# Performance work log

Measured on AMD Instinct MI355X. Metric: run time of the kernel, lower is better.

Reference implementation:

```python
import jax, jax.numpy as jnp
import numpy as np

N = 50000      # nodes
E = 800000     # edges
IN = 256       # in_feats
H = 128        # out_classes*2
OUT = 64       # out_classes
ALPHA = 0.3


def setup_inputs() -> dict:
    key = jax.random.key(0)
    ks = jax.random.split(key, 12)
    x = jax.random.normal(ks[0], (N, IN), jnp.float32)
    edge_index = jax.random.randint(ks[1], (2, E), 0, N, dtype=jnp.int32)
    def lin(k, fi, fo):
        s = 1.0 / np.float32(np.sqrt(fi))
        kw, kb = jax.random.split(k)
        return (jax.random.uniform(kw, (fi, fo), jnp.float32, -s, s),
                jax.random.uniform(kb, (fo,), jnp.float32, -s, s))
    W1, b1 = lin(ks[2], IN, H)
    W2, b2 = lin(ks[3], H, H)
    W3, b3 = lin(ks[4], H, H)
    Wfc, bfc = lin(ks[5], H, OUT)
    jk_weights = jax.random.normal(ks[6], (3,), jnp.float32)
    return dict(x=x, edge_index=edge_index, W1=W1, b1=b1, W2=W2, b2=b2,
                W3=W3, b3=b3, jk_weights=jk_weights, Wfc=Wfc, bfc=bfc)


def _gcn(x, W, b, src, dst, norm, n):
    # symmetric-normalized GCN conv with self-loops folded into src/dst/norm
    h = x @ W
    return jax.ops.segment_sum(norm[:, None] * h[src], dst, num_segments=n) + b


def reference(x, edge_index, W1, b1, W2, b2, W3, b3, jk_weights, Wfc, bfc):
    n = x.shape[0]
    row, col = edge_index[0], edge_index[1]
    loops = jnp.arange(n, dtype=edge_index.dtype)
    src = jnp.concatenate([row, loops])
    dst = jnp.concatenate([col, loops])
    deg = jax.ops.segment_sum(jnp.ones(src.shape, jnp.float32), dst, num_segments=n)
    dinv = jax.lax.rsqrt(jnp.maximum(deg, 1.0))  # deg >= 1 due to self-loops
    norm = dinv[src] * dinv[dst]

    layer_out = []
    # layer 0 + neighbor sampling (defaults make it exact out-neighbor mean)
    h = jax.nn.relu(_gcn(x, W1, b1, src, dst, norm, n))
    odeg = jax.ops.segment_sum(jnp.ones(row.shape, jnp.float32), row, num_segments=n)
    nsum = jax.ops.segment_sum(h[col], row, num_segments=n)
    h = jnp.where(odeg[:, None] > 0, nsum / jnp.maximum(odeg, 1.0)[:, None], h)
    layer_out.append(h)

    # layer 1 + historical EMA (fresh hist = detached x -> value identity, grad*alpha)
    h = jax.nn.relu(_gcn(h, W2, b2, src, dst, norm, n))
    sg = jax.lax.stop_gradient(h)
    h = sg + ALPHA * (h - sg)
    layer_out.append(h)

    # layer 2
    h = jax.nn.relu(_gcn(h, W3, b3, src, dst, norm, n))
    layer_out.append(h)

    w = jax.nn.softmax(jk_weights)
    jk = w[0] * layer_out[0] + w[1] * layer_out[1] + w[2] * layer_out[2]
    return jk @ Wfc + bfc
```

## Files before the change

### kernel.cpp

```cpp
#include <hip/hip_runtime.h>
#include <hip/hip_bf16.h>


#define H_FEATS 128
#define TPAD 136

typedef __attribute__((ext_vector_type(8))) short short8;
typedef __attribute__((ext_vector_type(4))) float float4v;
typedef unsigned short u16;

__device__ __forceinline__ float dload(const void* p, size_t i, int isbf) {
    return isbf ? __bfloat162float(((const __hip_bfloat16*)p)[i])
                : ((const float*)p)[i];
}

__device__ __forceinline__ float4 load4bf(const u16* p) {
    uint2 u = *(const uint2*)p;
    float4 f;
    f.x = __uint_as_float((u.x & 0xFFFFu) << 16);
    f.y = __uint_as_float(u.x & 0xFFFF0000u);
    f.z = __uint_as_float((u.y & 0xFFFFu) << 16);
    f.w = __uint_as_float(u.y & 0xFFFF0000u);
    return f;
}

__device__ __forceinline__ float bf2f(u16 h) {
    return __uint_as_float((unsigned)h << 16);
}

__device__ __forceinline__ u16 f2bf(float v) {
    return __bfloat16_as_ushort(__float2bfloat16(v));
}

__device__ __forceinline__ void add8(float* a, uint4 u) {
    a[0] += __uint_as_float((u.x & 0xFFFFu) << 16);
    a[1] += __uint_as_float(u.x & 0xFFFF0000u);
    a[2] += __uint_as_float((u.y & 0xFFFFu) << 16);
    a[3] += __uint_as_float(u.y & 0xFFFF0000u);
    a[4] += __uint_as_float((u.z & 0xFFFFu) << 16);
    a[5] += __uint_as_float(u.z & 0xFFFF0000u);
    a[6] += __uint_as_float((u.w & 0xFFFFu) << 16);
    a[7] += __uint_as_float(u.w & 0xFFFF0000u);
}

__device__ __forceinline__ void set8(float* a, uint4 u) {
    a[0] = __uint_as_float((u.x & 0xFFFFu) << 16);
    a[1] = __uint_as_float(u.x & 0xFFFF0000u);
    a[2] = __uint_as_float((u.y & 0xFFFFu) << 16);
    a[3] = __uint_as_float(u.y & 0xFFFF0000u);
    a[4] = __uint_as_float((u.z & 0xFFFFu) << 16);
    a[5] = __uint_as_float(u.z & 0xFFFF0000u);
    a[6] = __uint_as_float((u.w & 0xFFFFu) << 16);
    a[7] = __uint_as_float(u.w & 0xFFFF0000u);
}

__device__ __forceinline__ uint4 pack8(const float* f) {
    uint4 r;
    r.x = (unsigned)f2bf(f[0]) | ((unsigned)f2bf(f[1]) << 16);
    r.y = (unsigned)f2bf(f[2]) | ((unsigned)f2bf(f[3]) << 16);
    r.z = (unsigned)f2bf(f[4]) | ((unsigned)f2bf(f[5]) << 16);
    r.w = (unsigned)f2bf(f[6]) | ((unsigned)f2bf(f[7]) << 16);
    return r;
}

__device__ __forceinline__ void sniff_body(const unsigned int* __restrict__ x,
                                           const void* __restrict__ jkwb,
                                           float* __restrict__ meta) {
    __shared__ int cnt[256];
    int t = threadIdx.x;
    int c = 0;
    for (int i = 0; i < 16; i++) {
        unsigned int w = x[t * 16 + i];
        unsigned int e = (w >> 7) & 0xFFu;
        c += (e >= 0x60u && e <= 0x8Fu) ? 1 : 0;
    }
    cnt[t] = c;
    __syncthreads();
    for (int s = 128; s > 0; s >>= 1) {
        if (t < s) cnt[t] += cnt[t + s];
        __syncthreads();
    }
    if (t == 0) {
        int isbf = (cnt[0] > 3000) ? 1 : 0;
        ((int*)meta)[0] = isbf;
        float w0 = dload(jkwb, 0, isbf);
        float w1 = dload(jkwb, 1, isbf);
        float w2 = dload(jkwb, 2, isbf);
        float m = fmaxf(w0, fmaxf(w1, w2));
        float e0 = expf(w0 - m), e1 = expf(w1 - m), e2 = expf(w2 - m);
        float s = e0 + e1 + e2;
        meta[8] = e0 / s; meta[9] = e1 / s; meta[10] = e2 / s;
    }
}

__global__ __launch_bounds__(256) void sniff_jkw(const unsigned int* __restrict__ x,
                                                 const void* __restrict__ jkwb,
                                                 float* __restrict__ meta) {
    sniff_body(x, jkwb, meta);
}

#define CSR_CH 64
#define CSR_SL 8
#define CSR_NSC (CSR_CH * CSR_SL * 2)

__global__ __launch_bounds__(256) void count_partial(const int* __restrict__ row,
                                                     const int* __restrict__ col,
                                                     unsigned* __restrict__ partC,
                                                     unsigned* __restrict__ partR,
                                                     int E, int N,
                                                     const unsigned int* __restrict__ x,
                                                     const void* __restrict__ jkwb,
                                                     float* __restrict__ meta) {
    if (blockIdx.x == gridDim.x - 1) {
        sniff_body(x, jkwb, meta);
        return;
    }
    int b = blockIdx.x;
    int dir = b >> 9;
    int r = b & 511;
    int sl = r >> 6;
    int k  = r & 63;
    const int* arr = dir ? row : col;
    unsigned* part = (dir ? partR : partC) + (size_t)k * N;
    int lo = (int)(((long long)N * sl) >> 3);
    int hi = (int)(((long long)N * (sl + 1)) >> 3);
    int wid = hi - lo;

    __shared__ unsigned cnt[8192];
    for (int i = threadIdx.x; i < wid; i += 256) cnt[i] = 0;
    __syncthreads();

    int e0 = (int)(((long long)E * k) >> 6);
    int e1 = (int)(((long long)E * (k + 1)) >> 6);
    for (int e = e0 + threadIdx.x; e < e1; e += 256) {
        int d = arr[e] - lo;
        if ((unsigned)d < (unsigned)wid) atomicAdd(&cnt[d], 1u);
    }
    __syncthreads();
    for (int i = threadIdx.x; i < wid; i += 256) part[lo + i] = cnt[i];
}

__global__ __launch_bounds__(256) void reduce_bsum(const unsigned* __restrict__ partC,
                                                   const unsigned* __restrict__ partR,
                                                   int* __restrict__ cntc,
                                                   int* __restrict__ cntr,
                                                   int* __restrict__ b0,
                                                   int* __restrict__ b1, int N) {
    const unsigned* p = blockIdx.y ? partR : partC;
    int* cnt = blockIdx.y ? cntr : cntc;
    int* bs = blockIdx.y ? b1 : b0;
    int base = blockIdx.x * 1024 + threadIdx.x * 4;
    unsigned v0 = 0, v1 = 0, v2 = 0, v3 = 0;
    if (base + 3 < N) {
        for (int k = 0; k < CSR_CH; k++) {
            uint4 u = *(const uint4*)(p + (size_t)k * N + base);
            v0 += u.x; v1 += u.y; v2 += u.z; v3 += u.w;
        }
        int4 w = {(int)v0, (int)v1, (int)v2, (int)v3};
        *(int4*)&cnt[base] = w;
    } else {
        unsigned vv[4] = {0, 0, 0, 0};
        for (int k = 0; k < CSR_CH; k++)
            for (int i = 0; i < 4; i++)
                if (base + i < N) vv[i] += p[(size_t)k * N + base + i];
        for (int i = 0; i < 4; i++) if (base + i < N) cnt[base + i] = (int)vv[i];
        v0 = vv[0]; v1 = vv[1]; v2 = vv[2]; v3 = vv[3];
    }
    int s = (int)(v0 + v1 + v2 + v3);
    __shared__ int red[256];
    red[threadIdx.x] = s;
    __syncthreads();
    for (int d = 128; d > 0; d >>= 1) {
        if (threadIdx.x < d) red[threadIdx.x] += red[threadIdx.x + d];
        __syncthreads();
    }
    if (threadIdx.x == 0) bs[blockIdx.x] = red[0];
}

__device__ __forceinline__ void scatter_body(int b,
                                             const int* __restrict__ row,
                                             const int* __restrict__ col,
                                             const unsigned* __restrict__ partC,
                                             const unsigned* __restrict__ partR,
                                             u16* __restrict__ ecol,
                                             u16* __restrict__ erow,
                                             int E, int N,
                                             unsigned* __restrict__ cur) {
    int dir = b >> 9;
    int r = b & 511;
    int sl = r >> 6;
    int k  = r & 63;
    const int* darr = dir ? row : col;
    const int* sarr = dir ? col : row;
    u16* out = dir ? erow : ecol;
    const unsigned* base = (dir ? partR : partC) + (size_t)k * N;
    int lo = (int)(((long long)N * sl) >> 3);
    int hi = (int)(((long long)N * (sl + 1)) >> 3);
    int wid = hi - lo;

    for (int i = threadIdx.x; i < wid; i += 256) cur[i] = base[lo + i];
    __syncthreads();

    int e0 = (int)(((long long)E * k) >> 6);
    int e1 = (int)(((long long)E * (k + 1)) >> 6);
    for (int e = e0 + threadIdx.x; e < e1; e += 256) {
        int d = darr[e] - lo;
        if ((unsigned)d < (unsigned)wid) {
            unsigned p = atomicAdd(&cur[d], 1u);
            out[p] = (u16)sarr[e];
        }
    }
}

__global__ __launch_bounds__(256) void histo_sniff(const int* __restrict__ row, const int* __restrict__ col,
                                                   int* __restrict__ cntc, int* __restrict__ cntr, int E,
                                                   const unsigned int* __restrict__ x,
                                                   const void* __restrict__ jkwb,
                                                   float* __restrict__ meta) {
    if (blockIdx.x == gridDim.x - 1) {
        sniff_body(x, jkwb, meta);
        return;
    }
    int e = blockIdx.x * 256 + threadIdx.x;
    if (e < E) {
        atomicAdd(&cntc[col[e]], 1);
        atomicAdd(&cntr[row[e]], 1);
    }
}

__global__ __launch_bounds__(256) void scan_bsum(const int* __restrict__ c0, const int* __restrict__ c1,
                                                 int* __restrict__ b0, int* __restrict__ b1, int N) {
    const int* cnt = blockIdx.y ? c1 : c0;
    int* bs = blockIdx.y ? b1 : b0;
    int base = blockIdx.x * 1024 + threadIdx.x * 4;
    int s = 0;
    if (base + 3 < N) {
        int4 v = *(const int4*)&cnt[base];
        s = v.x + v.y + v.z + v.w;
    } else {
        for (int i = 0; i < 4; i++) if (base + i < N) s += cnt[base + i];
    }
    __shared__ int red[256];
    red[threadIdx.x] = s;
    __syncthreads();
    for (int d = 128; d > 0; d >>= 1) {
        if (threadIdx.x < d) red[threadIdx.x] += red[threadIdx.x + d];
        __syncthreads();
    }
    if (threadIdx.x == 0) bs[blockIdx.x] = red[0];
}

__global__ __launch_bounds__(256) void scan_bsum_scan(int* __restrict__ b0, int* __restrict__ b1,
                                                      int* __restrict__ offN0, int* __restrict__ offN1,
                                                      int nb) {
    int* bs = blockIdx.x ? b1 : b0;
    int* offN = blockIdx.x ? offN1 : offN0;
    __shared__ int sh[256];
    int t = threadIdx.x;
    int v = (t < nb) ? bs[t] : 0;
    sh[t] = v;
    __syncthreads();
    for (int d = 1; d < 256; d <<= 1) {
        int u = (t >= d) ? sh[t - d] : 0;
        __syncthreads();
        sh[t] += u;
        __syncthreads();
    }
    if (t < nb) bs[t] = (t == 0) ? 0 : sh[t - 1];
    if (t == 255) *offN = sh[255];
}

__global__ __launch_bounds__(256) void scan_final(const int* __restrict__ c0, const int* __restrict__ c1,
                                                  const int* __restrict__ b0, const int* __restrict__ b1,
                                                  int* __restrict__ o0, int* __restrict__ u0,
                                                  int* __restrict__ o1, int* __restrict__ u1,
                                                  unsigned* __restrict__ pc,
                                                  unsigned* __restrict__ pr,
                                                  float* __restrict__ dinvp, int N) {
    const int* cnt = blockIdx.y ? c1 : c0;
    const int* bs  = blockIdx.y ? b1 : b0;
    int* off = blockIdx.y ? o1 : o0;
    int* cur = blockIdx.y ? u1 : u0;
    unsigned* part = blockIdx.y ? pr : pc;
    int t = threadIdx.x;
    int base = blockIdx.x * 1024 + t * 4;
    int4 v = {0, 0, 0, 0};
    if (base + 3 < N) {
        v = *(const int4*)&cnt[base];
    } else {
        int tmp[4] = {0, 0, 0, 0};
        for (int i = 0; i < 4; i++) if (base + i < N) tmp[i] = cnt[base + i];
        v.x = tmp[0]; v.y = tmp[1]; v.z = tmp[2]; v.w = tmp[3];
    }
    if (blockIdx.y == 0) {
        if (base + 3 < N) {
            float4 dv;
            dv.x = rsqrtf(1.0f + (float)v.x);
            dv.y = rsqrtf(1.0f + (float)v.y);
            dv.z = rsqrtf(1.0f + (float)v.z);
            dv.w = rsqrtf(1.0f + (float)v.w);
            *(float4*)&dinvp[base] = dv;
        } else {
            int vv[4] = {v.x, v.y, v.z, v.w};
            for (int i = 0; i < 4; i++)
                if (base + i < N) dinvp[base + i] = rsqrtf(1.0f + (float)vv[i]);
        }
    }
    int s = v.x + v.y + v.z + v.w;
    __shared__ int sh[256];
    sh[t] = s;
    __syncthreads();
    for (int d = 1; d < 256; d <<= 1) {
        int u = (t >= d) ? sh[t - d] : 0;
        __syncthreads();
        sh[t] += u;
        __syncthreads();
    }
    int ex = bs[blockIdx.x] + ((t == 0) ? 0 : sh[t - 1]);
    int4 o;
    o.x = ex; o.y = ex + v.x; o.z = o.y + v.y; o.w = o.z + v.z;
    if (base + 3 < N) {
        *(int4*)&off[base] = o;
        *(int4*)&cur[base] = o;
        if (part) {
            unsigned a0 = (unsigned)o.x, a1 = (unsigned)o.y,
                     a2 = (unsigned)o.z, a3 = (unsigned)o.w;
            for (int k = 0; k < CSR_CH; k++) {
                unsigned* pp = part + (size_t)k * N + base;
                uint4 u = *(const uint4*)pp;
                uint4 w = {a0, a1, a2, a3};
                *(uint4*)pp = w;
                a0 += u.x; a1 += u.y; a2 += u.z; a3 += u.w;
            }
        }
    } else {
        int arr[4] = {o.x, o.y, o.z, o.w};
        for (int i = 0; i < 4; i++) if (base + i < N) { off[base + i] = arr[i]; cur[base + i] = arr[i]; }
        if (part) {
            for (int i = 0; i < 4; i++) {
                if (base + i >= N) continue;
                unsigned acc = (unsigned)arr[i];
                for (int k = 0; k < CSR_CH; k++) {
                    unsigned* pp = part + (size_t)k * N + base + i;
                    unsigned tv = *pp;
                    *pp = acc;
                    acc += tv;
                }
            }
        }
    }
}

__global__ __launch_bounds__(256) void scatter_tile(const int* __restrict__ row, const int* __restrict__ col,
                                                    int* __restrict__ curc, int* __restrict__ curr,
                                                    u16* __restrict__ ecol, u16* __restrict__ erow,
                                                    int E, int lo, int hi, int doRow) {
    int e = blockIdx.x * 256 + threadIdx.x;
    if (e >= E) return;
    int s = row[e], d = col[e];
    if (d >= lo && d < hi) {
        int p = atomicAdd(&curc[d], 1);
        ecol[p] = (u16)s;
    }
    if (doRow && s >= lo && s < hi) {
        int q = atomicAdd(&curr[s], 1);
        erow[q] = (u16)d;
    }
}

__global__ __launch_bounds__(256) void pack_all(const void* __restrict__ W1,
                                                const void* __restrict__ W2,
                                                const void* __restrict__ W3,
                                                const void* __restrict__ Wf,
                                                u16* __restrict__ Wp1,
                                                u16* __restrict__ Wp2,
                                                u16* __restrict__ Wp3,
                                                u16* __restrict__ Wfp,
                                                const int* __restrict__ flagp) {
    int bid = blockIdx.x;
    const void* W; u16* Wp; int K, C, gid;
    if (bid < 16)      { W = W1; Wp = Wp1; K = 256; C = 128; gid = bid * 256 + threadIdx.x; }
    else if (bid < 24) { W = W2; Wp = Wp2; K = 128; C = 128; gid = (bid - 16) * 256 + threadIdx.x; }
    else if (bid < 32) { W = W3; Wp = Wp3; K = 128; C = 128; gid = (bid - 24) * 256 + threadIdx.x; }
    else               { W = Wf; Wp = Wfp; K = 128; C = 64;  gid = (bid - 32) * 256 + threadIdx.x; }
    int tiles = C >> 4;
    int steps = K >> 5;
    if (gid >= steps * tiles * 64) return;
    int isbf = *flagp;
    int lane = gid & 63;
    int tt = (gid >> 6) % tiles;
    int s = (gid >> 6) / tiles;
    int krow = s * 32 + ((lane >> 4) << 3);
    int ncol = tt * 16 + (lane & 15);
#pragma unroll
    for (int j = 0; j < 8; j++) {
        float v = dload(W, (size_t)(krow + j) * C + ncol, isbf);
        Wp[(size_t)gid * 8 + j] = f2bf(v);
    }
}

template <int K, bool RTBF, bool BFIN, bool SCALE>
__device__ __forceinline__ void gemm_mfma_body(int bid, const void* __restrict__ Xv,
                                               const u16* __restrict__ Wp,
                                               u16* __restrict__ Cb,
                                               const float* __restrict__ dinv,
                                               const int* __restrict__ flagp, int M) {
    const int isbf = RTBF ? *flagp : (BFIN ? 1 : 0);
    const int tid = threadIdx.x;
    const int wave = tid >> 6, lane = tid & 63;
    const int m16 = lane & 15, quad = lane >> 4;
    const int row = bid * 64 + wave * 16 + m16;
    constexpr int STEPS = K / 32;

    float4v acc[8];
#pragma unroll
    for (int t = 0; t < 8; t++) acc[t] = (float4v){0.f, 0.f, 0.f, 0.f};

    const bool rowOK = row < M;
#pragma unroll
    for (int s = 0; s < STEPS; s++) {
        int k0 = s * 32 + quad * 8;
        short8 a = (short8)(short)0;
        if (rowOK) {
            if (isbf) {
                a = *(const short8*)((const u16*)Xv + (size_t)row * K + k0);
            } else {
                const float* p = (const float*)Xv + (size_t)row * K + k0;
                float4 f0 = *(const float4*)p;
                float4 f1 = *(const float4*)(p + 4);
                a[0] = (short)f2bf(f0.x); a[1] = (short)f2bf(f0.y);
                a[2] = (short)f2bf(f0.z); a[3] = (short)f2bf(f0.w);
                a[4] = (short)f2bf(f1.x); a[5] = (short)f2bf(f1.y);
                a[6] = (short)f2bf(f1.z); a[7] = (short)f2bf(f1.w);
            }
        }
#pragma unroll
        for (int t = 0; t < 8; t++) {
            short8 b = *(const short8*)(Wp + ((size_t)(s * 8 + t) * 64 + lane) * 8);
            acc[t] = __builtin_amdgcn_mfma_f32_16x16x32_bf16(a, b, acc[t], 0, 0, 0);
        }
    }
#pragma unroll
    for (int r = 0; r < 4; r++) {
        int gr = bid * 64 + wave * 16 + quad * 4 + r;
        if (gr < M) {
            float sc = SCALE ? dinv[gr] : 1.0f;
#pragma unroll
            for (int t = 0; t < 8; t++) {
                size_t o = (size_t)gr * H_FEATS + t * 16 + m16;
                Cb[o] = f2bf(sc * acc[t][r]);
            }
        }
    }
}

template <int K, bool RTBF, bool BFIN, bool SCALE>
__global__ __launch_bounds__(256) void gemm_mfma(const void* __restrict__ Xv,
                                                 const u16* __restrict__ Wp,
                                                 u16* __restrict__ Cb,
                                                 const float* __restrict__ dinv,
                                                 const int* __restrict__ flagp, int M) {
    gemm_mfma_body<K, RTBF, BFIN, SCALE>(blockIdx.x, Xv, Wp, Cb, dinv, flagp, M);
}

__global__ __launch_bounds__(256) void scatter_gemm0(const int* __restrict__ row,
                                                     const int* __restrict__ col,
                                                     const unsigned* __restrict__ partC,
                                                     const unsigned* __restrict__ partR,
                                                     u16* __restrict__ ecol,
                                                     u16* __restrict__ erow,
                                                     int E, int N,
                                                     const void* __restrict__ Xv,
                                                     const u16* __restrict__ Wp,
                                                     u16* __restrict__ Pb,
                                                     const float* __restrict__ dinv,
                                                     const int* __restrict__ flagp) {
    __shared__ unsigned cur[8192];
    if (blockIdx.x < CSR_NSC) {
        scatter_body(blockIdx.x, row, col, partC, partR, ecol, erow, E, N, cur);
    } else {
        gemm_mfma_body<256, true, false, true>(blockIdx.x - CSR_NSC, Xv, Wp, Pb, dinv, flagp, N);
    }
}

__global__ __launch_bounds__(256) void agg_sum(const int* __restrict__ off,
                                               const u16* __restrict__ idx,
                                               const float* __restrict__ dinv,
                                               const u16* __restrict__ Pb,
                                               const void* __restrict__ bv,
                                               u16* __restrict__ hout,
                                               const int* __restrict__ flagp, int N) {
    int node = blockIdx.x * 8 + (threadIdx.x >> 5);
    if (node >= N) return;
    int l = threadIdx.x & 31;
    int isbf = *flagp;
    int beg = off[node], end = off[node + 1];
    size_t ro = (size_t)l * 4;

    float4 acc = load4bf(&Pb[(size_t)node * H_FEATS + ro]);

    const float4 z = {0.f, 0.f, 0.f, 0.f};
    int i = beg;
    int s0 = (i     < end) ? (int)idx[i]     : 0;
    int s1 = (i + 1 < end) ? (int)idx[i + 1] : 0;
    int s2 = (i + 2 < end) ? (int)idx[i + 2] : 0;
    int s3 = (i + 3 < end) ? (int)idx[i + 3] : 0;
    float4 h0 = (i     < end) ? load4bf(&Pb[(size_t)s0 * H_FEATS + ro]) : z;
    float4 h1 = (i + 1 < end) ? load4bf(&Pb[(size_t)s1 * H_FEATS + ro]) : z;
    float4 h2 = (i + 2 < end) ? load4bf(&Pb[(size_t)s2 * H_FEATS + ro]) : z;
    float4 h3 = (i + 3 < end) ? load4bf(&Pb[(size_t)s3 * H_FEATS + ro]) : z;
    for (; i + 4 < end; i += 4) {
        int t0 = (int)idx[i + 4];
        int t1 = (i + 5 < end) ? (int)idx[i + 5] : 0;
        int t2 = (i + 6 < end) ? (int)idx[i + 6] : 0;
        int t3 = (i + 7 < end) ? (int)idx[i + 7] : 0;
        float4 n0 = load4bf(&Pb[(size_t)t0 * H_FEATS + ro]);
        float4 n1 = (i + 5 < end) ? load4bf(&Pb[(size_t)t1 * H_FEATS + ro]) : z;
        float4 n2 = (i + 6 < end) ? load4bf(&Pb[(size_t)t2 * H_FEATS + ro]) : z;
        float4 n3 = (i + 7 < end) ? load4bf(&Pb[(size_t)t3 * H_FEATS + ro]) : z;
        acc.x += (h0.x + h1.x) + (h2.x + h3.x);
        acc.y += (h0.y + h1.y) + (h2.y + h3.y);
        acc.z += (h0.z + h1.z) + (h2.z + h3.z);
        acc.w += (h0.w + h1.w) + (h2.w + h3.w);
        h0 = n0; h1 = n1; h2 = n2; h3 = n3;
    }
    acc.x += (h0.x + h1.x) + (h2.x + h3.x);
    acc.y += (h0.y + h1.y) + (h2.y + h3.y);
    acc.z += (h0.z + h1.z) + (h2.z + h3.z);
    acc.w += (h0.w + h1.w) + (h2.w + h3.w);

    float dd = dinv[node];
    acc.x = fmaxf(fmaf(dd, acc.x, dload(bv, l * 4 + 0, isbf)), 0.0f);
    acc.y = fmaxf(fmaf(dd, acc.y, dload(bv, l * 4 + 1, isbf)), 0.0f);
    acc.z = fmaxf(fmaf(dd, acc.z, dload(bv, l * 4 + 2, isbf)), 0.0f);
    acc.w = fmaxf(fmaf(dd, acc.w, dload(bv, l * 4 + 3, isbf)), 0.0f);
    uint2 pk;
    pk.x = (unsigned)f2bf(acc.x) | ((unsigned)f2bf(acc.y) << 16);
    pk.y = (unsigned)f2bf(acc.z) | ((unsigned)f2bf(acc.w) << 16);
    *(uint2*)&hout[(size_t)node * H_FEATS + ro] = pk;
}

template <int MODE, bool WRITEG>
__device__ __forceinline__ void gather_tile(int bid,
                                            const int* __restrict__ off,
                                            const u16* __restrict__ idx,
                                            const float* __restrict__ dinv,
                                            const u16* __restrict__ Src,
                                            const void* __restrict__ bv, int isbf,
                                            u16* __restrict__ Hg,
                                            u16* __restrict__ tile, int N) {
    int lane16 = threadIdx.x & 15;
    int rloc = threadIdx.x >> 4;
    int co = lane16 * 8;
    const uint4 zz = {0u, 0u, 0u, 0u};
#pragma unroll
    for (int pass = 0; pass < 4; ++pass) {
        int r = pass * 16 + rloc;
        int gr = bid * 64 + r;
        uint4* ldst = (uint4*)(tile + (size_t)r * TPAD + co);
        if (gr >= N) { *ldst = zz; continue; }
        int beg = off[gr], end = off[gr + 1];
        float acc[8];
        if (MODE == 0) {
            uint4 u = *(const uint4*)(Src + (size_t)gr * H_FEATS + co);
            set8(acc, u);
        } else {
#pragma unroll
            for (int j = 0; j < 8; j++) acc[j] = 0.0f;
        }
        int i = beg;
        int s0 = (i     < end) ? (int)idx[i]     : 0;
        int s1 = (i + 1 < end) ? (int)idx[i + 1] : 0;
        int s2 = (i + 2 < end) ? (int)idx[i + 2] : 0;
        int s3 = (i + 3 < end) ? (int)idx[i + 3] : 0;
        uint4 h0 = (i     < end) ? *(const uint4*)(Src + (size_t)s0 * H_FEATS + co) : zz;
        uint4 h1 = (i + 1 < end) ? *(const uint4*)(Src + (size_t)s1 * H_FEATS + co) : zz;
        uint4 h2 = (i + 2 < end) ? *(const uint4*)(Src + (size_t)s2 * H_FEATS + co) : zz;
        uint4 h3 = (i + 3 < end) ? *(const uint4*)(Src + (size_t)s3 * H_FEATS + co) : zz;
        for (; i + 4 < end; i += 4) {
            int t0 = (int)idx[i + 4];
            int t1 = (i + 5 < end) ? (int)idx[i + 5] : 0;
            int t2 = (i + 6 < end) ? (int)idx[i + 6] : 0;
            int t3 = (i + 7 < end) ? (int)idx[i + 7] : 0;
            uint4 n0 = *(const uint4*)(Src + (size_t)t0 * H_FEATS + co);
            uint4 n1 = (i + 5 < end) ? *(const uint4*)(Src + (size_t)t1 * H_FEATS + co) : zz;
            uint4 n2 = (i + 6 < end) ? *(const uint4*)(Src + (size_t)t2 * H_FEATS + co) : zz;
            uint4 n3 = (i + 7 < end) ? *(const uint4*)(Src + (size_t)t3 * H_FEATS + co) : zz;
            add8(acc, h0); add8(acc, h1); add8(acc, h2); add8(acc, h3);
            h0 = n0; h1 = n1; h2 = n2; h3 = n3;
        }
        add8(acc, h0); add8(acc, h1); add8(acc, h2); add8(acc, h3);

        if (MODE == 0) {
            float dd = dinv[gr];
#pragma unroll
            for (int j = 0; j < 8; j++)
                acc[j] = fmaxf(fmaf(dd, acc[j], dload(bv, co + j, isbf)), 0.0f);
        } else {
            int cnt = end - beg;
            if (cnt > 0) {
                float inv = 1.0f / (float)cnt;
#pragma unroll
                for (int j = 0; j < 8; j++) acc[j] *= inv;
            } else {
                uint4 u = *(const uint4*)(Src + (size_t)gr * H_FEATS + co);
                set8(acc, u);
            }
        }
        uint4 pk = pack8(acc);
        *ldst = pk;
        if (WRITEG) *(uint4*)(Hg + (size_t)gr * H_FEATS + co) = pk;
    }
}

__device__ __forceinline__ void gemm_lds_body(int bid, const u16* __restrict__ tile,
                                              const u16* __restrict__ Wp,
                                              u16* __restrict__ Cb,
                                              const float* __restrict__ dinv, int M) {
    const int tid = threadIdx.x;
    const int wave = tid >> 6, lane = tid & 63;
    const int m16 = lane & 15, quad = lane >> 4;
    const int lrow = wave * 16 + m16;

    float4v acc[8];
#pragma unroll
    for (int t = 0; t < 8; t++) acc[t] = (float4v){0.f, 0.f, 0.f, 0.f};

#pragma unroll
    for (int s = 0; s < 4; s++) {
        int k0 = s * 32 + quad * 8;
        short8 a = *(const short8*)(tile + (size_t)lrow * TPAD + k0);
#pragma unroll
        for (int t = 0; t < 8; t++) {
            short8 b = *(const short8*)(Wp + ((size_t)(s * 8 + t) * 64 + lane) * 8);
            acc[t] = __builtin_amdgcn_mfma_f32_16x16x32_bf16(a, b, acc[t], 0, 0, 0);
        }
    }
#pragma unroll
    for (int r = 0; r < 4; r++) {
        int gr = bid * 64 + wave * 16 + quad * 4 + r;
        if (gr < M) {
            float sc = dinv[gr];
#pragma unroll
            for (int t = 0; t < 8; t++) {
                size_t o = (size_t)gr * H_FEATS + t * 16 + m16;
                Cb[o] = f2bf(sc * acc[t][r]);
            }
        }
    }
}

template <int MODE>
__global__ __launch_bounds__(256) void agg_gemm(const int* __restrict__ off,
                                                const u16* __restrict__ idx,
                                                const float* __restrict__ dinv,
                                                const u16* __restrict__ Src,
                                                const void* __restrict__ bv,
                                                const u16* __restrict__ Wp,
                                                u16* __restrict__ Hg,
                                                u16* __restrict__ Pnext,
                                                const int* __restrict__ flagp, int N) {
    __shared__ u16 tile[64 * TPAD];
    gather_tile<MODE, true>(blockIdx.x, off, idx, dinv, Src, bv, *flagp, Hg, tile, N);
    __syncthreads();
    gemm_lds_body(blockIdx.x, tile, Wp, Pnext, dinv, N);
}

__global__ __launch_bounds__(256) void agg_fc3(const int* __restrict__ off,
                                               const u16* __restrict__ idx,
                                               const float* __restrict__ dinv,
                                               const u16* __restrict__ Src,
                                               const void* __restrict__ bv3,
                                               const u16* __restrict__ H0,
                                               const u16* __restrict__ H1,
                                               const u16* __restrict__ Wfp,
                                               const void* __restrict__ bv,
                                               void* __restrict__ Outv,
                                               const float* __restrict__ meta, int N) {
    __shared__ u16 tile[64 * TPAD];
    const int isbf = ((const int*)meta)[0];
    gather_tile<0, false>(blockIdx.x, off, idx, dinv, Src, bv3, isbf, (u16*)0, tile, N);
    __syncthreads();

    const float w0 = meta[8], w1 = meta[9], w2 = meta[10];
    const int tid = threadIdx.x;
    const int wave = tid >> 6, lane = tid & 63;
    const int m16 = lane & 15, quad = lane >> 4;
    const int lrow = wave * 16 + m16;
    const int gr0 = blockIdx.x * 64 + lrow;

    float4v acc[4];
#pragma unroll
    for (int t = 0; t < 4; t++) acc[t] = (float4v){0.f, 0.f, 0.f, 0.f};

#pragma unroll
    for (int s = 0; s < 4; s++) {
        int k0 = s * 32 + quad * 8;
        short8 a = (short8)(short)0;
        if (gr0 < N) {
            float f0[8], f1[8], f2[8];
            uint4 u0 = *(const uint4*)(H0 + (size_t)gr0 * H_FEATS + k0);
            uint4 u1 = *(const uint4*)(H1 + (size_t)gr0 * H_FEATS + k0);
            uint4 tv = *(const uint4*)(tile + (size_t)lrow * TPAD + k0);
            set8(f0, u0); set8(f1, u1); set8(f2, tv);
#pragma unroll
            for (int j = 0; j < 8; j++)
                a[j] = (short)f2bf(w0 * f0[j] + w1 * f1[j] + w2 * f2[j]);
        }
#pragma unroll
        for (int t = 0; t < 4; t++) {
            short8 b = *(const short8*)(Wfp + ((size_t)(s * 4 + t) * 64 + lane) * 8);
            acc[t] = __builtin_amdgcn_mfma_f32_16x16x32_bf16(a, b, acc[t], 0, 0, 0);
        }
    }

    __hip_bfloat16* ob = (__hip_bfloat16*)Outv;
    float* of = (float*)Outv;
#pragma unroll
    for (int r = 0; r < 4; r++) {
        int gr = blockIdx.x * 64 + wave * 16 + quad * 4 + r;
        if (gr < N) {
#pragma unroll
            for (int t = 0; t < 4; t++) {
                int c = t * 16 + m16;
                size_t o = (size_t)gr * 64 + c;
                float v = acc[t][r] + dload(bv, c, isbf);
                if (isbf) ob[o] = __float2bfloat16(v); else of[o] = v;
            }
        }
    }
}

template <bool BF16OUT>
__global__ __launch_bounds__(256) void agg_gather3b(const int* __restrict__ off,
                                                    const u16* __restrict__ idx,
                                                    const float* __restrict__ dinv,
                                                    const u16* __restrict__ Hb,
                                                    const void* __restrict__ bv,
                                                    void* __restrict__ houtv,
                                                    const int* __restrict__ flagp, int N) {
    int node = blockIdx.x * 8 + (threadIdx.x >> 5);
    if (node >= N) return;
    int l = threadIdx.x & 31;
    int isbf = *flagp;
    int beg = off[node], end = off[node + 1];
    float dd = dinv[node];
    size_t ro = (size_t)l * 4;

    float4 self = load4bf(&Hb[(size_t)node * H_FEATS + ro]);
    float w0s = dd * dd;
    float4 acc = {w0s * self.x, w0s * self.y, w0s * self.z, w0s * self.w};

    int i = beg;
    int s0 = (i < end) ? (int)idx[i] : 0;
    float4 h0 = (i < end) ? load4bf(&Hb[(size_t)s0 * H_FEATS + ro])
                          : (float4){0.f, 0.f, 0.f, 0.f};
    for (; i < end; i++) {
        int s1 = (i + 1 < end) ? (int)idx[i + 1] : 0;
        float4 h1 = (i + 1 < end) ? load4bf(&Hb[(size_t)s1 * H_FEATS + ro]) : h0;
        float w = dinv[s0] * dd;
        acc.x = fmaf(w, h0.x, acc.x);
        acc.y = fmaf(w, h0.y, acc.y);
        acc.z = fmaf(w, h0.z, acc.z);
        acc.w = fmaf(w, h0.w, acc.w);
        s0 = s1; h0 = h1;
    }
    acc.x = fmaxf(acc.x + dload(bv, l * 4 + 0, isbf), 0.0f);
    acc.y = fmaxf(acc.y + dload(bv, l * 4 + 1, isbf), 0.0f);
    acc.z = fmaxf(acc.z + dload(bv, l * 4 + 2, isbf), 0.0f);
    acc.w = fmaxf(acc.w + dload(bv, l * 4 + 3, isbf), 0.0f);
    if (BF16OUT) {
        u16* hb = (u16*)houtv;
        uint2 pk;
        pk.x = (unsigned)f2bf(acc.x) | ((unsigned)f2bf(acc.y) << 16);
        pk.y = (unsigned)f2bf(acc.z) | ((unsigned)f2bf(acc.w) << 16);
        *(uint2*)&hb[(size_t)node * H_FEATS + ro] = pk;
    } else {
        *(float4*)&((float*)houtv)[(size_t)node * H_FEATS + ro] = acc;
    }
}

template <int K, bool XIN, bool GATEBF, bool BF16OUT>
__global__ __launch_bounds__(256) void gemm128(const void* __restrict__ Xv,
                                               const void* __restrict__ Wv,
                                               void* __restrict__ Cv,
                                               const int* __restrict__ flagp, int N) {
    constexpr int BM = 64, BK = 16, BN = 128, TN = 8, TX = BN / TN;
    __shared__ float Xs[BK][BM + 4];
    __shared__ float Ws[BK][BN];
    const int isbf = *flagp;
    if (GATEBF && isbf != 1) return;
    const float* Xf = (const float*)Xv;

    const int tid = threadIdx.x;
    const int tx = tid % TX;
    const int ty = tid / TX;
    const int rowBase = blockIdx.x * BM;

    float acc[4][TN] = {};
    const int lk = tid % BK;
    const int lr0 = tid / BK;

    for (int kb = 0; kb < K; kb += BK) {
#pragma unroll
        for (int i = 0; i < 4; i++) {
            int r = lr0 + i * 16;
            int gr = rowBase + r;
            float v = 0.0f;
            if (gr < N) {
                size_t idx = (size_t)gr * K + kb + lk;
                v = XIN ? dload(Xv, idx, isbf) : Xf[idx];
            }
            Xs[lk][r] = v;
        }
#pragma unroll
        for (int i = 0; i < 8; i++) {
            int idx = i * 256 + tid;
            int k = idx >> 7, c = idx & 127;
            Ws[k][c] = dload(Wv, (size_t)(kb + k) * BN + c, isbf);
        }
        __syncthreads();
#pragma unroll
        for (int k = 0; k < BK; k++) {
            float4 a = *(const float4*)&Xs[k][ty * 4];
            float av[4] = {a.x, a.y, a.z, a.w};
            float4 b0 = *(const float4*)&Ws[k][tx * TN];
            float4 b1 = *(const float4*)&Ws[k][tx * TN + 4];
            float bv[8] = {b0.x, b0.y, b0.z, b0.w, b1.x, b1.y, b1.z, b1.w};
#pragma unroll
            for (int i = 0; i < 4; i++)
#pragma unroll
                for (int j = 0; j < TN; j++) acc[i][j] = fmaf(av[i], bv[j], acc[i][j]);
        }
        __syncthreads();
    }
#pragma unroll
    for (int i = 0; i < 4; i++) {
        int gr = rowBase + ty * 4 + i;
        if (gr < N) {
#pragma unroll
            for (int j = 0; j < TN; j++) {
                size_t o = (size_t)gr * BN + tx * TN + j;
                if (BF16OUT) ((u16*)Cv)[o] = f2bf(acc[i][j]);
                else         ((float*)Cv)[o] = acc[i][j];
            }
        }
    }
}

template <bool FIRST, bool LAST, bool BFIN>
__global__ __launch_bounds__(256) void fc_accum(const void* __restrict__ Hmv,
                                                const void* __restrict__ Wv,
                                                const void* __restrict__ bv,
                                                void* __restrict__ Outv,
                                                const float* __restrict__ meta,
                                                int widx, int N) {
    constexpr int BM = 64, BK = 16, BN = 64, TN = 4, TX = BN / TN, K = 128;
    __shared__ float Xs[BK][BM + 4];
    __shared__ float Ws[BK][BN];
    const int isbf = ((const int*)meta)[0];
    const float scale = meta[8 + widx];

    const int tid = threadIdx.x;
    const int tx = tid % TX;
    const int ty = tid / TX;
    const int rowBase = blockIdx.x * BM;

    float acc[4][TN] = {};
    const int lk = tid % BK;
    const int lr0 = tid / BK;

    for (int kb = 0; kb < K; kb += BK) {
#pragma unroll
        for (int i = 0; i < 4; i++) {
            int r = lr0 + i * 16;
            int gr = rowBase + r;
            float v = 0.0f;
            if (gr < N) {
                size_t idx = (size_t)gr * K + kb + lk;
                if (BFIN) v = bf2f(((const u16*)Hmv)[idx]);
                else      v = ((const float*)Hmv)[idx];
            }
            Xs[lk][r] = v;
        }
#pragma unroll
        for (int i = 0; i < 4; i++) {
            int idx = i * 256 + tid;
            int k = idx >> 6, c = idx & 63;
            Ws[k][c] = dload(Wv, (size_t)(kb + k) * BN + c, isbf);
        }
        __syncthreads();
#pragma unroll
        for (int k = 0; k < BK; k++) {
            float4 a = *(const float4*)&Xs[k][ty * 4];
            float av[4] = {a.x, a.y, a.z, a.w};
            float4 bb = *(const float4*)&Ws[k][tx * TN];
            float bvv[4] = {bb.x, bb.y, bb.z, bb.w};
#pragma unroll
            for (int i = 0; i < 4; i++)
#pragma unroll
                for (int j = 0; j < TN; j++) acc[i][j] = fmaf(av[i], bvv[j], acc[i][j]);
        }
        __syncthreads();
    }
    __hip_bfloat16* ob = (__hip_bfloat16*)Outv;
    float* of = (float*)Outv;
#pragma unroll
    for (int i = 0; i < 4; i++) {
        int gr = rowBase + ty * 4 + i;
        if (gr < N) {
#pragma unroll
            for (int j = 0; j < TN; j++) {
                int c = tx * TN + j;
                size_t o = (size_t)gr * BN + c;
                float v = scale * acc[i][j];
                if (!FIRST) v += isbf ? __bfloat162float(ob[o]) : of[o];
                if (LAST) v += dload(bv, c, isbf);
                if (isbf) ob[o] = __float2bfloat16(v); else of[o] = v;
            }
        }
    }
}

__global__ __launch_bounds__(256) void init_deg(float* deg, float* odeg, int N) {
    int i = blockIdx.x * 256 + threadIdx.x;
    if (i < N) { deg[i] = 1.0f; odeg[i] = 0.0f; }
}
__global__ __launch_bounds__(256) void count_deg(const int* __restrict__ row, const int* __restrict__ col,
                                                 float* deg, float* odeg, int E) {
    int e = blockIdx.x * 256 + threadIdx.x;
    if (e < E) {
        atomicAdd(&deg[col[e]], 1.0f);
        atomicAdd(&odeg[row[e]], 1.0f);
    }
}
__global__ __launch_bounds__(256) void deg_to_dinv(float* deg, int N) {
    int i = blockIdx.x * 256 + threadIdx.x;
    if (i < N) deg[i] = rsqrtf(deg[i]);
}
__global__ __launch_bounds__(256) void agg_edges(const int* __restrict__ row, const int* __restrict__ col,
                                                 const float* __restrict__ dinv,
                                                 const float* __restrict__ H,
                                                 float* __restrict__ agg, int E) {
    int e = blockIdx.x * 2 + (threadIdx.x >> 7);
    if (e >= E) return;
    int j = threadIdx.x & 127;
    int s = row[e], d = col[e];
    float w = dinv[s] * dinv[d];
    atomicAdd(&agg[(size_t)d * H_FEATS + j], w * H[(size_t)s * H_FEATS + j]);
}
__global__ __launch_bounds__(256) void mean_edges(const int* __restrict__ row, const int* __restrict__ col,
                                                  const float* __restrict__ h0pre,
                                                  float* __restrict__ nsum, int E) {
    int e = blockIdx.x * 2 + (threadIdx.x >> 7);
    if (e >= E) return;
    int j = threadIdx.x & 127;
    int r = row[e], c = col[e];
    atomicAdd(&nsum[(size_t)r * H_FEATS + j], h0pre[(size_t)c * H_FEATS + j]);
}
__global__ __launch_bounds__(256) void finalize_layer(const float* __restrict__ agg,
                                                      const float* __restrict__ H,
                                                      const float* __restrict__ dinv,
                                                      const void* __restrict__ bv,
                                                      float* __restrict__ hout,
                                                      const int* __restrict__ flagp, int NH) {
    int idx = blockIdx.x * 256 + threadIdx.x;
    if (idx >= NH) return;
    int isbf = *flagp;
    int v = idx >> 7, j = idx & 127;
    float di = dinv[v];
    float h = fmaf(di * di, H[idx], agg[idx]) + dload(bv, j, isbf);
    hout[idx] = fmaxf(h, 0.0f);
}
__global__ __launch_bounds__(256) void finalize_mean(const float* __restrict__ nsum,
                                                     const float* __restrict__ h0pre,
                                                     const float* __restrict__ odeg,
                                                     float* __restrict__ h0, int NH) {
    int idx = blockIdx.x * 256 + threadIdx.x;
    if (idx >= NH) return;
    int v = idx >> 7;
    float od = odeg[v];
    h0[idx] = (od > 0.0f) ? (nsum[idx] / od) : h0pre[idx];
}
__global__ __launch_bounds__(256) void finalize_mean_cnt(const float* __restrict__ nsum,
                                                         const float* __restrict__ h0pre,
                                                         const int* __restrict__ cntr,
                                                         float* __restrict__ h0, int NH) {
    int idx = blockIdx.x * 256 + threadIdx.x;
    if (idx >= NH) return;
    int v = idx >> 7;
    int od = cntr[v];
    h0[idx] = (od > 0) ? (nsum[idx] / (float)od) : h0pre[idx];
}

extern "C" void kernel_launch(void* const* d_in, const int* in_sizes, int n_in,
                              void* d_out, int out_size, void* d_ws, size_t ws_size,
                              hipStream_t stream) {
    const void* x   = d_in[0];
    const int*  ei  = (const int*)d_in[1];
    const void* W1  = d_in[2];
    const void* b1  = d_in[3];
    const void* W2  = d_in[4];
    const void* b2  = d_in[5];
    const void* W3  = d_in[6];
    const void* b3  = d_in[7];
    const void* jkb = d_in[8];
    const void* Wfc = d_in[9];
    const void* bfc = d_in[10];

    const int IN = 256;
    const int N = in_sizes[0] / IN;
    const int E = in_sizes[1] / 2;
    const int NH = N * H_FEATS;

    const int* row = ei;
    const int* col = ei + E;

    auto a4 = [](size_t v) { return (v + 3) & ~(size_t)3; };
    float* ws = (float*)d_ws;
    size_t o = 0;
    float* meta  = ws + o;           o += 256;
    float* dinv  = ws + o;           o += N;          o = a4(o);
    int*   cntc  = (int*)(ws + o);   o += N;          o = a4(o);
    int*   cntr  = (int*)(ws + o);   o += N;          o = a4(o);
    int*   bsumc = (int*)(ws + o);   o += 256;
    int*   bsumr = (int*)(ws + o);   o += 256;
    int*   coff  = (int*)(ws + o);   o += N + 1;      o = a4(o);
    int*   curc  = (int*)(ws + o);   o += N;          o = a4(o);
    u16*   ecol  = (u16*)(ws + o);   o += E;          o = a4(o);
    size_t oB_small = o;
    int*   roff  = (int*)(ws + o);   o += N + 1;      o = a4(o);
    int*   curr  = (int*)(ws + o);   o += N;          o = a4(o);
    u16*   erow  = (u16*)(ws + o);   o += E;          o = a4(o);
    size_t oA_full = o;

    auto alignup = [](size_t v) { return (v + 63) & ~(size_t)63; };
    const size_t WPW = 16384 + 8192 + 8192 + 4096;
    size_t needA = alignup(oA_full) + 2 * (size_t)NH + 64 + WPW;
    size_t needB = alignup(oB_small) + 2 * (size_t)NH + 64 + WPW;

    int tier;
    size_t hoff;
    if (N >= 65536)                { tier = 2; hoff = alignup(256 + 2 * (size_t)N); }
    else if (ws_size >= needA * 4) { tier = 0; hoff = alignup(oA_full); }
    else if (ws_size >= needB * 4) { tier = 1; hoff = alignup(oB_small); }
    else                           { tier = 2; hoff = alignup(256 + 2 * (size_t)N); }
    float* A = ws + hoff;
    float* B = A + NH;
    u16* HbA = (u16*)A;
    u16* HbB = (u16*)B;
    u16* Pb  = (u16*)A;
    u16* Qb  = Pb + (size_t)NH;
    u16* H0b = Pb + 2 * (size_t)NH;
    u16* H1b = Pb + 3 * (size_t)NH;
    unsigned* partC = (unsigned*)H0b;
    unsigned* partR = partC + (size_t)CSR_CH * N;
    size_t wpoff = alignup(hoff + 2 * (size_t)NH);
    u16* Wp1 = (u16*)(ws + wpoff);
    u16* Wp2 = Wp1 + 32768;
    u16* Wp3 = Wp2 + 16384;
    u16* Wfcp = Wp3 + 16384;
    float* odegf = ws + 256 + N;
    const int* flag = (const int*)meta;

    dim3 blk(256);
    int gN = (N + 255) / 256;
    int gE = (E + 255) / 256;
    int gE2 = (E + 1) / 2;
    int gNH = (NH + 255) / 256;
    int gGemm = (N + 63) / 64;
    int gNode8 = (N + 7) / 8;
    int nb = (N + 1023) / 1024;

    if (tier == 0) {
        count_partial<<<CSR_NSC + 1, blk, 0, stream>>>(row, col, partC, partR, E, N,
                                                       (const unsigned int*)x, jkb, meta);
        pack_all<<<36, blk, 0, stream>>>(W1, W2, W3, Wfc, Wp1, Wp2, Wp3, Wfcp, flag);
        reduce_bsum<<<dim3(nb, 2), blk, 0, stream>>>(partC, partR, cntc, cntr, bsumc, bsumr, N);
        scan_bsum_scan<<<2, blk, 0, stream>>>(bsumc, bsumr, &coff[N], &roff[N], nb);
        scan_final<<<dim3(nb, 2), blk, 0, stream>>>(cntc, cntr, bsumc, bsumr,
                                                    coff, curc, roff, curr,
                                                    partC, partR, dinv, N);

        scatter_gemm0<<<CSR_NSC + gGemm, blk, 0, stream>>>(row, col, partC, partR, ecol, erow,
                                                           E, N, x, Wp1, Pb, dinv, flag);

        agg_sum<<<gNode8, blk, 0, stream>>>(coff, ecol, dinv, Pb, b1, Qb, flag, N);

        agg_gemm<1><<<gGemm, blk, 0, stream>>>(roff, erow, dinv, Qb, b1, Wp2, H0b, Pb, flag, N);

        agg_gemm<0><<<gGemm, blk, 0, stream>>>(coff, ecol, dinv, Pb, b2, Wp3, H1b, Qb, flag, N);

        agg_fc3<<<gGemm, blk, 0, stream>>>(coff, ecol, dinv, Qb, b3, H0b, H1b,
                                           Wfcp, bfc, d_out, meta, N);
    } else if (tier == 1) {
        hipMemsetAsync(cntc, 0, 2 * (size_t)N * 4, stream);
        histo_sniff<<<gE + 1, blk, 0, stream>>>(row, col, cntc, cntr, E,
                                                (const unsigned int*)x, jkb, meta);
        const int T = 4;
        int step = (N + T - 1) / T;
        scan_bsum<<<dim3(nb, 1), blk, 0, stream>>>(cntc, cntc, bsumc, bsumc, N);
        scan_bsum_scan<<<1, blk, 0, stream>>>(bsumc, bsumc, &coff[N], &coff[N], nb);
        scan_final<<<dim3(nb, 1), blk, 0, stream>>>(cntc, cntc, bsumc, bsumc,
                                                    coff, curc, coff, curc,
                                                    (unsigned*)0, (unsigned*)0, dinv, N);
        for (int t = 0; t < T; t++) {
            int lo = t * step, hi = lo + step; if (hi > N) hi = N;
            scatter_tile<<<gE, blk, 0, stream>>>(row, col, curc, curc, ecol, ecol, E, lo, hi, 0);
        }

        pack_all<<<36, blk, 0, stream>>>(W1, W2, W3, Wfc, Wp1, Wp2, Wp3, Wfcp, flag);

        gemm_mfma<256, true, false, false><<<gGemm, blk, 0, stream>>>(x, Wp1, HbA, dinv, flag, N);
        agg_gather3b<false><<<gNode8, blk, 0, stream>>>(coff, ecol, dinv, HbA, b1, B, flag, N);
        hipMemsetAsync(A, 0, (size_t)NH * 4, stream);
        mean_edges<<<gE2, blk, 0, stream>>>(row, col, B, A, E);
        finalize_mean_cnt<<<gNH, blk, 0, stream>>>(A, B, cntr, A, NH);
        fc_accum<true, false, false><<<gGemm, blk, 0, stream>>>(A, Wfc, bfc, d_out, meta, 0, N);

        gemm_mfma<128, false, false, false><<<gGemm, blk, 0, stream>>>(A, Wp2, HbB, dinv, flag, N);
        agg_gather3b<true><<<gNode8, blk, 0, stream>>>(coff, ecol, dinv, HbB, b2, HbA, flag, N);
        fc_accum<false, false, true><<<gGemm, blk, 0, stream>>>(HbA, Wfc, bfc, d_out, meta, 1, N);

        gemm_mfma<128, false, true, false><<<gGemm, blk, 0, stream>>>(HbA, Wp3, HbB, dinv, flag, N);
        agg_gather3b<true><<<gNode8, blk, 0, stream>>>(coff, ecol, dinv, HbB, b3, HbA, flag, N);
        fc_accum<false, true, true><<<gGemm, blk, 0, stream>>>(HbA, Wfc, bfc, d_out, meta, 2, N);
    } else {
        sniff_jkw<<<1, blk, 0, stream>>>((const unsigned int*)x, jkb, meta);
        init_deg<<<gN, blk, 0, stream>>>(dinv, odegf, N);
        count_deg<<<gE, blk, 0, stream>>>(row, col, dinv, odegf, E);
        deg_to_dinv<<<gN, blk, 0, stream>>>(dinv, N);

        gemm128<256, true, false, false><<<gGemm, blk, 0, stream>>>(x, W1, A, flag, N);
        hipMemsetAsync(B, 0, (size_t)NH * 4, stream);
        agg_edges<<<gE2, blk, 0, stream>>>(row, col, dinv, A, B, E);
        finalize_layer<<<gNH, blk, 0, stream>>>(B, A, dinv, b1, B, flag, NH);
        hipMemsetAsync(A, 0, (size_t)NH * 4, stream);
        mean_edges<<<gE2, blk, 0, stream>>>(row, col, B, A, E);
        finalize_mean<<<gNH, blk, 0, stream>>>(A, B, odegf, A, NH);
        fc_accum<true, false, false><<<gGemm, blk, 0, stream>>>(A, Wfc, bfc, d_out, meta, 0, N);

        gemm128<128, false, false, false><<<gGemm, blk, 0, stream>>>(A, W2, B, flag, N);
        hipMemsetAsync(A, 0, (size_t)NH * 4, stream);
        agg_edges<<<gE2, blk, 0, stream>>>(row, col, dinv, B, A, E);
        finalize_layer<<<gNH, blk, 0, stream>>>(A, B, dinv, b2, A, flag, NH);
        fc_accum<false, false, false><<<gGemm, blk, 0, stream>>>(A, Wfc, bfc, d_out, meta, 1, N);

        gemm128<128, false, false, false><<<gGemm, blk, 0, stream>>>(A, W3, B, flag, N);
        hipMemsetAsync(A, 0, (size_t)NH * 4, stream);
        agg_edges<<<gE2, blk, 0, stream>>>(row, col, dinv, B, A, E);
        finalize_layer<<<gNH, blk, 0, stream>>>(A, B, dinv, b3, A, flag, NH);
        fc_accum<false, true, false><<<gGemm, blk, 0, stream>>>(A, Wfc, bfc, d_out, meta, 2, N);
    }
}
```

Baseline: 405.8 us.

## Halve fused gather-GEMM tile to 32 rows and size CSR LDS dynamically

```diff
diff --git a/kernel.cpp b/kernel.cpp
--- a/kernel.cpp
+++ b/kernel.cpp
@@ -115,6 +115,7 @@
         sniff_body(x, jkwb, meta);
         return;
     }
+    extern __shared__ unsigned cnt[];
     int b = blockIdx.x;
     int dir = b >> 9;
     int r = b & 511;
@@ -126,7 +127,6 @@
     int hi = (int)(((long long)N * (sl + 1)) >> 3);
     int wid = hi - lo;
 
-    __shared__ unsigned cnt[8192];
     for (int i = threadIdx.x; i < wid; i += 256) cnt[i] = 0;
     __syncthreads();
 
@@ -475,7 +475,7 @@
                                                      u16* __restrict__ Pb,
                                                      const float* __restrict__ dinv,
                                                      const int* __restrict__ flagp) {
-    __shared__ unsigned cur[8192];
+    extern __shared__ unsigned cur[];
     if (blockIdx.x < CSR_NSC) {
         scatter_body(blockIdx.x, row, col, partC, partR, ecol, erow, E, N, cur);
     } else {
@@ -554,9 +554,9 @@
     int co = lane16 * 8;
     const uint4 zz = {0u, 0u, 0u, 0u};
 #pragma unroll
-    for (int pass = 0; pass < 4; ++pass) {
+    for (int pass = 0; pass < 2; ++pass) {
         int r = pass * 16 + rloc;
-        int gr = bid * 64 + r;
+        int gr = bid * 32 + r;
         uint4* ldst = (uint4*)(tile + (size_t)r * TPAD + co);
         if (gr >= N) { *ldst = zz; continue; }
         int beg = off[gr], end = off[gr + 1];
@@ -613,37 +613,39 @@
     }
 }
 
-__device__ __forceinline__ void gemm_lds_body(int bid, const u16* __restrict__ tile,
-                                              const u16* __restrict__ Wp,
-                                              u16* __restrict__ Cb,
-                                              const float* __restrict__ dinv, int M) {
+__device__ __forceinline__ void gemm_lds_body32(int bid, const u16* __restrict__ tile,
+                                                const u16* __restrict__ Wp,
+                                                u16* __restrict__ Cb,
+                                                const float* __restrict__ dinv, int M) {
     const int tid = threadIdx.x;
     const int wave = tid >> 6, lane = tid & 63;
     const int m16 = lane & 15, quad = lane >> 4;
-    const int lrow = wave * 16 + m16;
-
-    float4v acc[8];
-#pragma unroll
-    for (int t = 0; t < 8; t++) acc[t] = (float4v){0.f, 0.f, 0.f, 0.f};
+    const int rg = wave & 1, cg = wave >> 1;
+    const int lrow = rg * 16 + m16;
+
+    float4v acc[4];
+#pragma unroll
+    for (int t = 0; t < 4; t++) acc[t] = (float4v){0.f, 0.f, 0.f, 0.f};
 
 #pragma unroll
     for (int s = 0; s < 4; s++) {
         int k0 = s * 32 + quad * 8;
         short8 a = *(const short8*)(tile + (size_t)lrow * TPAD + k0);
 #pragma unroll
-        for (int t = 0; t < 8; t++) {
-            short8 b = *(const short8*)(Wp + ((size_t)(s * 8 + t) * 64 + lane) * 8);
+        for (int t = 0; t < 4; t++) {
+            int tg = cg * 4 + t;
+            short8 b = *(const short8*)(Wp + ((size_t)(s * 8 + tg) * 64 + lane) * 8);
             acc[t] = __builtin_amdgcn_mfma_f32_16x16x32_bf16(a, b, acc[t], 0, 0, 0);
         }
     }
 #pragma unroll
     for (int r = 0; r < 4; r++) {
-        int gr = bid * 64 + wave * 16 + quad * 4 + r;
+        int gr = bid * 32 + rg * 16 + quad * 4 + r;
         if (gr < M) {
             float sc = dinv[gr];
 #pragma unroll
-            for (int t = 0; t < 8; t++) {
-                size_t o = (size_t)gr * H_FEATS + t * 16 + m16;
+            for (int t = 0; t < 4; t++) {
+                size_t o = (size_t)gr * H_FEATS + (cg * 4 + t) * 16 + m16;
                 Cb[o] = f2bf(sc * acc[t][r]);
             }
         }
@@ -660,10 +662,10 @@
                                                 u16* __restrict__ Hg,
                                                 u16* __restrict__ Pnext,
                                                 const int* __restrict__ flagp, int N) {
-    __shared__ u16 tile[64 * TPAD];
+    __shared__ u16 tile[32 * TPAD];
     gather_tile<MODE, true>(blockIdx.x, off, idx, dinv, Src, bv, *flagp, Hg, tile, N);
     __syncthreads();
-    gemm_lds_body(blockIdx.x, tile, Wp, Pnext, dinv, N);
+    gemm_lds_body32(blockIdx.x, tile, Wp, Pnext, dinv, N);
 }
 
 __global__ __launch_bounds__(256) void agg_fc3(const int* __restrict__ off,
@@ -677,7 +679,7 @@
                                                const void* __restrict__ bv,
                                                void* __restrict__ Outv,
                                                const float* __restrict__ meta, int N) {
-    __shared__ u16 tile[64 * TPAD];
+    __shared__ u16 tile[32 * TPAD];
     const int isbf = ((const int*)meta)[0];
     gather_tile<0, false>(blockIdx.x, off, idx, dinv, Src, bv3, isbf, (u16*)0, tile, N);
     __syncthreads();
@@ -686,12 +688,13 @@
     const int tid = threadIdx.x;
     const int wave = tid >> 6, lane = tid & 63;
     const int m16 = lane & 15, quad = lane >> 4;
-    const int lrow = wave * 16 + m16;
-    const int gr0 = blockIdx.x * 64 + lrow;
-
-    float4v acc[4];
-#pragma unroll
-    for (int t = 0; t < 4; t++) acc[t] = (float4v){0.f, 0.f, 0.f, 0.f};
+    const int rg = wave & 1, cg = wave >> 1;
+    const int lrow = rg * 16 + m16;
+    const int gr0 = blockIdx.x * 32 + lrow;
+
+    float4v acc[2];
+#pragma unroll
+    for (int t = 0; t < 2; t++) acc[t] = (float4v){0.f, 0.f, 0.f, 0.f};
 
 #pragma unroll
     for (int s = 0; s < 4; s++) {
@@ -708,8 +711,9 @@
                 a[j] = (short)f2bf(w0 * f0[j] + w1 * f1[j] + w2 * f2[j]);
         }
 #pragma unroll
-        for (int t = 0; t < 4; t++) {
-            short8 b = *(const short8*)(Wfp + ((size_t)(s * 4 + t) * 64 + lane) * 8);
+        for (int t = 0; t < 2; t++) {
+            int tg = cg * 2 + t;
+            short8 b = *(const short8*)(Wfp + ((size_t)(s * 4 + tg) * 64 + lane) * 8);
             acc[t] = __builtin_amdgcn_mfma_f32_16x16x32_bf16(a, b, acc[t], 0, 0, 0);
         }
     }
@@ -718,11 +722,11 @@
     float* of = (float*)Outv;
 #pragma unroll
     for (int r = 0; r < 4; r++) {
-        int gr = blockIdx.x * 64 + wave * 16 + quad * 4 + r;
+        int gr = blockIdx.x * 32 + rg * 16 + quad * 4 + r;
         if (gr < N) {
 #pragma unroll
-            for (int t = 0; t < 4; t++) {
-                int c = t * 16 + m16;
+            for (int t = 0; t < 2; t++) {
+                int c = (cg * 2 + t) * 16 + m16;
                 size_t o = (size_t)gr * 64 + c;
                 float v = acc[t][r] + dload(bv, c, isbf);
                 if (isbf) ob[o] = __float2bfloat16(v); else of[o] = v;
@@ -1069,12 +1073,14 @@
     int gE2 = (E + 1) / 2;
     int gNH = (NH + 255) / 256;
     int gGemm = (N + 63) / 64;
+    int gG32 = (N + 31) / 32;
     int gNode8 = (N + 7) / 8;
     int nb = (N + 1023) / 1024;
+    size_t shb = (size_t)((N + CSR_SL - 1) / CSR_SL) * 4;
 
     if (tier == 0) {
-        count_partial<<<CSR_NSC + 1, blk, 0, stream>>>(row, col, partC, partR, E, N,
-                                                       (const unsigned int*)x, jkb, meta);
+        count_partial<<<CSR_NSC + 1, blk, shb, stream>>>(row, col, partC, partR, E, N,
+                                                         (const unsigned int*)x, jkb, meta);
         pack_all<<<36, blk, 0, stream>>>(W1, W2, W3, Wfc, Wp1, Wp2, Wp3, Wfcp, flag);
         reduce_bsum<<<dim3(nb, 2), blk, 0, stream>>>(partC, partR, cntc, cntr, bsumc, bsumr, N);
         scan_bsum_scan<<<2, blk, 0, stream>>>(bsumc, bsumr, &coff[N], &roff[N], nb);
@@ -1082,17 +1088,17 @@
                                                     coff, curc, roff, curr,
                                                     partC, partR, dinv, N);
 
-        scatter_gemm0<<<CSR_NSC + gGemm, blk, 0, stream>>>(row, col, partC, partR, ecol, erow,
-                                                           E, N, x, Wp1, Pb, dinv, flag);
+        scatter_gemm0<<<CSR_NSC + gGemm, blk, shb, stream>>>(row, col, partC, partR, ecol, erow,
+                                                             E, N, x, Wp1, Pb, dinv, flag);
 
         agg_sum<<<gNode8, blk, 0, stream>>>(coff, ecol, dinv, Pb, b1, Qb, flag, N);
 
-        agg_gemm<1><<<gGemm, blk, 0, stream>>>(roff, erow, dinv, Qb, b1, Wp2, H0b, Pb, flag, N);
-
-        agg_gemm<0><<<gGemm, blk, 0, stream>>>(coff, ecol, dinv, Pb, b2, Wp3, H1b, Qb, flag, N);
-
-        agg_fc3<<<gGemm, blk, 0, stream>>>(coff, ecol, dinv, Qb, b3, H0b, H1b,
-                                           Wfcp, bfc, d_out, meta, N);
+        agg_gemm<1><<<gG32, blk, 0, stream>>>(roff, erow, dinv, Qb, b1, Wp2, H0b, Pb, flag, N);
+
+        agg_gemm<0><<<gG32, blk, 0, stream>>>(coff, ecol, dinv, Pb, b2, Wp3, H1b, Qb, flag, N);
+
+        agg_fc3<<<gG32, blk, 0, stream>>>(coff, ecol, dinv, Qb, b3, H0b, H1b,
+                                          Wfcp, bfc, d_out, meta, N);
     } else if (tier == 1) {
         hipMemsetAsync(cntc, 0, 2 * (size_t)N * 4, stream);
         histo_sniff<<<gE + 1, blk, 0, stream>>>(row, col, cntc, cntr, E,
```

Result: faster. 396.8 us (-2.2%).
